# Kernel optimization log

Hardware: AMD Instinct MI355X
Metric: run time of the kernel (lower is better)

Reference implementation:

```python
import jax, jax.numpy as jnp
import numpy as np

HIDDEN = 4096
N_HEADS = 8
HEAD = HIDDEN // N_HEADS  # 512
SCALE = float(HIDDEN) ** 0.5  # NOTE: module MULTIPLIES by sqrt(hidden_dim), faithful to source
NEG = -1e9


def setup_inputs() -> dict:
    key = jax.random.key(0)
    ks = jax.random.split(key, 7)
    B, S = 4, 2048
    q = jax.random.normal(ks[0], (B, S, HIDDEN), dtype=jnp.float32)
    k = jax.random.normal(ks[1], (B, S, HIDDEN), dtype=jnp.float32)
    v = jax.random.normal(ks[2], (B, S, HIDDEN), dtype=jnp.float32)
    mask = jax.random.randint(ks[3], (B, S), 0, 2, dtype=jnp.int32)
    w_std = 1.0 / np.sqrt(HIDDEN)
    Wq = jax.random.normal(ks[4], (HEAD, HIDDEN), dtype=jnp.float32) * w_std
    Wk = jax.random.normal(ks[5], (HEAD, HIDDEN), dtype=jnp.float32) * w_std
    Wv = jax.random.normal(ks[6], (HEAD, HIDDEN), dtype=jnp.float32) * w_std
    return {"q": q, "k": k, "v": v, "mask": mask, "Wq": Wq, "Wk": Wk, "Wv": Wv}


def reference(q, k, v, mask, Wq, Wk, Wv):
    # bias-free linear projections (nn.Linear: x @ W.T)
    qh = jnp.einsum('bse,de->bsd', q, Wq)  # [B,S,HEAD]
    kh = jnp.einsum('bse,de->bsd', k, Wk)
    vh = jnp.einsum('bse,de->bsd', v, Wv)
    # scores: q @ k^T, then MULTIPLY by sqrt(hidden_dim) as in source
    scores = jnp.einsum('bsd,btd->bst', qh, kh) * SCALE  # [B,S,S]
    # additive mask over keys: mask [B,S] -> [B,1,S]; done under no_grad in torch
    scores = jnp.where(mask[:, None, :] == 0, NEG, scores)
    scores = jax.lax.stop_gradient(scores)  # torch no_grad reassignment detaches
    attn = jax.nn.softmax(scores, axis=-1)
    # dropout p=0.0 -> identity
    out = jnp.einsum('bst,btd->bsd', attn, vh)  # [B,S,HEAD]
    return out
```

## Files before the change

kernel.cpp:

```cpp
#include <hip/hip_runtime.h>

#define HIDDEN 4096
#define HEADD  512
#define SEQ    2048
#define NBATCH 4
#define KSPLIT 4
#define KRANGE (SEQ/KSPLIT)
#define KSTR   520

typedef float f32x4 __attribute__((ext_vector_type(4)));
typedef short s16x8 __attribute__((ext_vector_type(8)));

__device__ __forceinline__ unsigned short f2bf(float x){
  unsigned u = __float_as_uint(x);
  u += 0x7fffu + ((u >> 16) & 1u);
  return (unsigned short)(u >> 16);
}
__device__ __forceinline__ float bf2f(unsigned short b){
  return __uint_as_float(((unsigned)b) << 16);
}
__device__ __forceinline__ void gl_lds16(const unsigned short* g, unsigned short* l){
  __builtin_amdgcn_global_load_lds((const __attribute__((address_space(1))) unsigned int*)g,
                                   (__attribute__((address_space(3))) unsigned int*)l,
                                   16, 0, 0);
}

__global__ void wsplit_kernel(const float* __restrict__ Wq,
                              const float* __restrict__ Wk,
                              const float* __restrict__ Wv,
                              unsigned short* __restrict__ wqh, unsigned short* __restrict__ wql,
                              unsigned short* __restrict__ wkh, unsigned short* __restrict__ wkl,
                              unsigned short* __restrict__ wvh){
  const int n4 = HEADD * HIDDEN / 4;
  for (int i = blockIdx.x * blockDim.x + threadIdx.x; i < n4; i += gridDim.x * blockDim.x){
    float4 a = ((const float4*)Wq)[i];
    ushort4 h, lo;
    h.x = f2bf(a.x); lo.x = f2bf(a.x - bf2f(h.x));
    h.y = f2bf(a.y); lo.y = f2bf(a.y - bf2f(h.y));
    h.z = f2bf(a.z); lo.z = f2bf(a.z - bf2f(h.z));
    h.w = f2bf(a.w); lo.w = f2bf(a.w - bf2f(h.w));
    ((ushort4*)wqh)[i] = h; ((ushort4*)wql)[i] = lo;
    a = ((const float4*)Wk)[i];
    h.x = f2bf(a.x); lo.x = f2bf(a.x - bf2f(h.x));
    h.y = f2bf(a.y); lo.y = f2bf(a.y - bf2f(h.y));
    h.z = f2bf(a.z); lo.z = f2bf(a.z - bf2f(h.z));
    h.w = f2bf(a.w); lo.w = f2bf(a.w - bf2f(h.w));
    ((ushort4*)wkh)[i] = h; ((ushort4*)wkl)[i] = lo;
    a = ((const float4*)Wv)[i];
    h.x = f2bf(a.x); h.y = f2bf(a.y); h.z = f2bf(a.z); h.w = f2bf(a.w);
    ((ushort4*)wvh)[i] = h;
  }
}

__global__ __launch_bounds__(512, 4)
void proj_all_kernel(const float* __restrict__ q, const float* __restrict__ k,
                     const float* __restrict__ v,
                     const unsigned short* __restrict__ wqh, const unsigned short* __restrict__ wql,
                     const unsigned short* __restrict__ wkh, const unsigned short* __restrict__ wkl,
                     const unsigned short* __restrict__ wvh,
                     unsigned short* __restrict__ qhh, unsigned short* __restrict__ qhl,
                     unsigned short* __restrict__ khh, unsigned short* __restrict__ khl,
                     unsigned short* __restrict__ vhT){
  __shared__ unsigned short Ah[2][128*32];
  __shared__ unsigned short Al[2*128*32];
  __shared__ unsigned short Bh[2][128*32];
  __shared__ unsigned short Bl[2*128*32];

  const int tid  = threadIdx.x;
  const int lane = tid & 63, wid = tid >> 6;
  const int quad = lane >> 4, l16 = lane & 15;
  const int wm = wid >> 1, wn = wid & 1;

  const int wg  = blockIdx.x + 4 * blockIdx.y + 256 * blockIdx.z;
  const int lwg = (wg & 7) * 96 + (wg >> 3);
  const int n0 = (lwg & 3) * 128;
  const int m0 = ((lwg >> 2) & 63) * 128;
  const int z  = lwg >> 8;

  const float* X = (z == 0) ? q : (z == 1) ? k : v;
  const unsigned short* Wh = (z == 0) ? wqh : (z == 1) ? wkh : wvh;
  const unsigned short* Wl = (z == 0) ? wql : (z == 1) ? wkl : wvh;
  unsigned short* Ohi = (z == 0) ? qhh : khh;
  unsigned short* Olo = (z == 0) ? qhl : khl;
  const bool full = (z < 2);

  const int sB    = (lane & 7) ^ (lane >> 3);
  const int browS = ((lane >> 3) << 1) + (sB >> 2);
  const int bcolS = (sB & 3) << 3;

  const int fbase = ((l16 >> 1) << 6) + ((((((l16 & 1) << 2) | quad)) ^ (l16 >> 1)) << 3);

  f32x4 acc[2][4];
  #pragma unroll
  for (int i = 0; i < 2; i++)
    #pragma unroll
    for (int j = 0; j < 4; j++){
      f32x4 zz = {0.f, 0.f, 0.f, 0.f};
      acc[i][j] = zz;
    }

  float4 xa[4];
  int ar[4], ahalf[4], acin[4], aidx[4];
  #pragma unroll
  for (int c = 0; c < 4; c++){
    int chunk = tid + c * 512;
    ar[c]    = chunk >> 4;
    int col4 = (chunk & 15) << 2;
    ahalf[c] = col4 >> 5;
    acin[c]  = col4 & 31;
    int R  = ar[c] >> 1;
    int sA = (((ar[c] & 1) << 2) | (acin[c] >> 3)) ^ (R & 7);
    aidx[c] = (R << 6) + (sA << 3) + (acin[c] & 7);
    xa[c] = *(const float4*)(X + (size_t)(m0 + ar[c]) * HIDDEN + col4);
  }

  for (int k0 = 0; k0 < HIDDEN; k0 += 64){
    #pragma unroll
    for (int c = 0; c < 4; c++){
      ushort4 hv;
      hv.x = f2bf(xa[c].x); hv.y = f2bf(xa[c].y); hv.z = f2bf(xa[c].z); hv.w = f2bf(xa[c].w);
      *(ushort4*)(&Ah[ahalf[c]][aidx[c]]) = hv;
      if (full){
        ushort4 lv;
        lv.x = f2bf(xa[c].x - bf2f(hv.x));
        lv.y = f2bf(xa[c].y - bf2f(hv.y));
        lv.z = f2bf(xa[c].z - bf2f(hv.z));
        lv.w = f2bf(xa[c].w - bf2f(hv.w));
        *(ushort4*)(&Al[ahalf[c]*4096 + aidx[c]]) = lv;
      }
    }
    #pragma unroll
    for (int h = 0; h < 2; h++){
      const unsigned short* gh = Wh + (size_t)(n0 + wid*16 + browS) * HIDDEN + k0 + h*32 + bcolS;
      gl_lds16(gh, &Bh[h][wid*512]);
      if (full){
        const unsigned short* gl = Wl + (size_t)(n0 + wid*16 + browS) * HIDDEN + k0 + h*32 + bcolS;
        gl_lds16(gl, &Bl[h*4096 + wid*512]);
      }
    }
    __syncthreads();
    if (k0 + 64 < HIDDEN){
      #pragma unroll
      for (int c = 0; c < 4; c++){
        int col4 = ahalf[c]*32 + acin[c];
        xa[c] = *(const float4*)(X + (size_t)(m0 + ar[c]) * HIDDEN + k0 + 64 + col4);
      }
    }
    #pragma unroll
    for (int h = 0; h < 2; h++){
      s16x8 ah[2], al[2], bh[4], bl[4];
      #pragma unroll
      for (int i = 0; i < 2; i++){
        ah[i] = *(const s16x8*)(&Ah[h][(wm*32 + i*16)*32 + fbase]);
        if (full) al[i] = *(const s16x8*)(&Al[h*4096 + (wm*32 + i*16)*32 + fbase]);
      }
      #pragma unroll
      for (int j = 0; j < 4; j++){
        bh[j] = *(const s16x8*)(&Bh[h][(wn*64 + j*16)*32 + fbase]);
        if (full) bl[j] = *(const s16x8*)(&Bl[h*4096 + (wn*64 + j*16)*32 + fbase]);
      }
      #pragma unroll
      for (int i = 0; i < 2; i++)
        #pragma unroll
        for (int j = 0; j < 4; j++){
          acc[i][j] = __builtin_amdgcn_mfma_f32_16x16x32_bf16(ah[i], bh[j], acc[i][j], 0, 0, 0);
          if (full){
            acc[i][j] = __builtin_amdgcn_mfma_f32_16x16x32_bf16(ah[i], bl[j], acc[i][j], 0, 0, 0);
            acc[i][j] = __builtin_amdgcn_mfma_f32_16x16x32_bf16(al[i], bh[j], acc[i][j], 0, 0, 0);
          }
        }
    }
    __syncthreads();
  }

  if (full){
    #pragma unroll
    for (int i = 0; i < 2; i++)
      #pragma unroll
      for (int j = 0; j < 4; j++)
        #pragma unroll
        for (int r = 0; r < 4; r++){
          int m = m0 + wm*32 + i*16 + quad*4 + r;
          int n = n0 + wn*64 + j*16 + l16;
          float c = acc[i][j][r];
          unsigned short h = f2bf(c);
          Ohi[(size_t)m * HEADD + n] = h;
          Olo[(size_t)m * HEADD + n] = f2bf(c - bf2f(h));
        }
  } else {
    #pragma unroll
    for (int i = 0; i < 2; i++)
      #pragma unroll
      for (int j = 0; j < 4; j++){
        int mbase = m0 + wm*32 + i*16 + quad*4;
        int d = n0 + wn*64 + j*16 + l16;
        int b = mbase >> 11;
        int t = mbase & 2047;
        ushort4 vv;
        vv.x = f2bf(acc[i][j][0]);
        vv.y = f2bf(acc[i][j][1]);
        vv.z = f2bf(acc[i][j][2]);
        vv.w = f2bf(acc[i][j][3]);
        *(ushort4*)(vhT + ((size_t)(b * HEADD + d)) * SEQ + t) = vv;
      }
  }
}

__global__ __launch_bounds__(512, 2)
void flash_kernel(const unsigned short* __restrict__ qhh, const unsigned short* __restrict__ qhl,
                  const unsigned short* __restrict__ khh, const unsigned short* __restrict__ khl,
                  const unsigned short* __restrict__ vhT, const int* __restrict__ mask,
                  float* __restrict__ part, float* __restrict__ ml){
  __shared__ unsigned short Kh[32*KSTR];
  __shared__ unsigned short Kl[32*KSTR];
  __shared__ unsigned short Vt[512*32];
  __shared__ unsigned short Pt[8*512];

  const int tid = threadIdx.x, lane = tid & 63, wid = tid >> 6;
  const int quad = lane >> 4, l16 = lane & 15;

  const int wg  = blockIdx.x + (int)gridDim.x * (blockIdx.y + (int)gridDim.y * blockIdx.z);
  const int lwg = (wg & 7) * 32 + (wg >> 3);
  const int qt = lwg & 15;
  const int kz = (lwg >> 4) & 3;
  const int b  = lwg >> 6;
  const int qrow0 = qt * 128 + wid * 16;
  const int kbase = kz * KRANGE;

  const int sV   = (lane & 7) ^ (lane >> 3);
  const int vdro = ((lane >> 3) << 1) + (sV >> 2);
  const int vcol = (sV & 3) << 3;
  const int vbase = ((l16 >> 1) << 6) + ((((((l16 & 1) << 2) | quad)) ^ (l16 >> 1)) << 3);

  const size_t qoff = ((size_t)(b * SEQ) + qrow0 + l16) * HEADD + quad * 8;
  s16x8 qh[16];
  #pragma unroll
  for (int ds = 0; ds < 16; ds++) qh[ds] = *(const s16x8*)(qhh + qoff + ds*32);

  float mrow[4], lrow[4];
  #pragma unroll
  for (int r = 0; r < 4; r++){ mrow[r] = -3.0e38f; lrow[r] = 0.f; }
  f32x4 oacc[32];
  #pragma unroll
  for (int j = 0; j < 32; j++){
    f32x4 z = {0.f, 0.f, 0.f, 0.f};
    oacc[j] = z;
  }

  auto stageK = [&](int kt){
    #pragma unroll
    for (int c = 0; c < 4; c++){
      int keyl = wid*4 + c;
      size_t g = ((size_t)(b * SEQ) + kbase + kt + keyl) * HEADD + lane*8;
      gl_lds16(khh + g, Kh + keyl*KSTR);
      gl_lds16(khl + g, Kl + keyl*KSTR);
    }
  };
  auto stageV = [&](int kt){
    #pragma unroll
    for (int c = 0; c < 4; c++){
      int d0 = wid*64 + c*16;
      const unsigned short* vs = vhT + ((size_t)(b * HEADD) + d0 + vdro) * SEQ
                                     + kbase + kt + vcol;
      gl_lds16(vs, Vt + d0*32);
    }
  };

  stageK(0);
  stageV(0);
  __syncthreads();

  for (int kt = 0; kt < KRANGE; kt += 32){
    const bool has_next = (kt + 32 < KRANGE);
    const int key0 = kbase + kt + l16;
    const int mk0 = mask[b * SEQ + key0];
    const int mk1 = mask[b * SEQ + key0 + 16];

    f32x4 s0 = {0.f,0.f,0.f,0.f}, s1 = {0.f,0.f,0.f,0.f};
    #pragma unroll
    for (int ds = 0; ds < 16; ds++){
      s16x8 aL  = *(const s16x8*)(qhl + qoff + ds*32);
      s16x8 b0H = *(const s16x8*)(Kh + l16*KSTR      + ds*32 + quad*8);
      s16x8 b0L = *(const s16x8*)(Kl + l16*KSTR      + ds*32 + quad*8);
      s16x8 b1H = *(const s16x8*)(Kh + (16+l16)*KSTR + ds*32 + quad*8);
      s16x8 b1L = *(const s16x8*)(Kl + (16+l16)*KSTR + ds*32 + quad*8);
      s0 = __builtin_amdgcn_mfma_f32_16x16x32_bf16(qh[ds], b0H, s0, 0, 0, 0);
      s0 = __builtin_amdgcn_mfma_f32_16x16x32_bf16(qh[ds], b0L, s0, 0, 0, 0);
      s0 = __builtin_amdgcn_mfma_f32_16x16x32_bf16(aL,     b0H, s0, 0, 0, 0);
      s0 = __builtin_amdgcn_mfma_f32_16x16x32_bf16(aL,     b0L, s0, 0, 0, 0);
      s1 = __builtin_amdgcn_mfma_f32_16x16x32_bf16(qh[ds], b1H, s1, 0, 0, 0);
      s1 = __builtin_amdgcn_mfma_f32_16x16x32_bf16(qh[ds], b1L, s1, 0, 0, 0);
      s1 = __builtin_amdgcn_mfma_f32_16x16x32_bf16(aL,     b1H, s1, 0, 0, 0);
      s1 = __builtin_amdgcn_mfma_f32_16x16x32_bf16(aL,     b1L, s1, 0, 0, 0);
    }

    __syncthreads();

    if (has_next) stageK(kt + 32);

    float sm0[4], sm1[4];
    #pragma unroll
    for (int r = 0; r < 4; r++){
      sm0[r] = mk0 ? s0[r] * 64.0f : -1.0e9f;
      sm1[r] = mk1 ? s1[r] * 64.0f : -1.0e9f;
    }
    float rm[4];
    #pragma unroll
    for (int r = 0; r < 4; r++) rm[r] = fmaxf(sm0[r], sm1[r]);
    #pragma unroll
    for (int sh = 1; sh < 16; sh <<= 1){
      #pragma unroll
      for (int r = 0; r < 4; r++) rm[r] = fmaxf(rm[r], __shfl_xor(rm[r], sh, 64));
    }
    bool needv = false;
    #pragma unroll
    for (int r = 0; r < 4; r++) needv = needv || (rm[r] > mrow[r] + 10.0f);
    const bool dorescale = (__any(needv ? 1 : 0) != 0);
    float alpha[4];
    if (dorescale){
      #pragma unroll
      for (int r = 0; r < 4; r++){
        float mn = fmaxf(mrow[r], rm[r]);
        alpha[r] = __expf(mrow[r] - mn);
        mrow[r] = mn;
      }
    } else {
      #pragma unroll
      for (int r = 0; r < 4; r++) alpha[r] = 1.0f;
    }
    float p0[4], p1[4], rs[4];
    #pragma unroll
    for (int r = 0; r < 4; r++){
      p0[r] = __expf(sm0[r] - mrow[r]);
      p1[r] = __expf(sm1[r] - mrow[r]);
      rs[r] = p0[r] + p1[r];
    }
    #pragma unroll
    for (int sh = 1; sh < 16; sh <<= 1){
      #pragma unroll
      for (int r = 0; r < 4; r++) rs[r] += __shfl_xor(rs[r], sh, 64);
    }
    #pragma unroll
    for (int r = 0; r < 4; r++) lrow[r] = lrow[r] * alpha[r] + rs[r];
    #pragma unroll
    for (int r = 0; r < 4; r++){
      Pt[wid*512 + (quad*4 + r)*32 + l16]      = f2bf(p0[r]);
      Pt[wid*512 + (quad*4 + r)*32 + 16 + l16] = f2bf(p1[r]);
    }
    if (dorescale){
      #pragma unroll
      for (int j = 0; j < 32; j++)
        #pragma unroll
        for (int r = 0; r < 4; r++) oacc[j][r] *= alpha[r];
    }
    s16x8 pa = *(const s16x8*)(Pt + wid*512 + l16*32 + quad*8);
    #pragma unroll
    for (int j = 0; j < 32; j++){
      s16x8 vb = *(const s16x8*)(Vt + j*512 + vbase);
      oacc[j] = __builtin_amdgcn_mfma_f32_16x16x32_bf16(pa, vb, oacc[j], 0, 0, 0);
    }

    __syncthreads();

    if (has_next) stageV(kt + 32);
  }

  const size_t prow = (size_t)(kz * (NBATCH*SEQ)) + b * SEQ + qrow0;
  #pragma unroll
  for (int j = 0; j < 32; j++)
    #pragma unroll
    for (int r = 0; r < 4; r++)
      part[(prow + quad*4 + r) * HEADD + j*16 + l16] = oacc[j][r];
  if (l16 == 0){
    #pragma unroll
    for (int r = 0; r < 4; r++){
      ml[(prow + quad*4 + r)*2 + 0] = mrow[r];
      ml[(prow + quad*4 + r)*2 + 1] = lrow[r];
    }
  }
}

__global__ __launch_bounds__(256)
void reduce_kernel(const float* __restrict__ part, const float* __restrict__ ml,
                   float* __restrict__ out){
  const int row = blockIdx.x;
  const int t = threadIdx.x;
  float m[KSPLIT], l[KSPLIT];
  float M = -3.0e38f;
  #pragma unroll
  for (int j = 0; j < KSPLIT; j++){
    m[j] = ml[((size_t)j*(NBATCH*SEQ) + row)*2 + 0];
    l[j] = ml[((size_t)j*(NBATCH*SEQ) + row)*2 + 1];
    M = fmaxf(M, m[j]);
  }
  float w[KSPLIT], L = 0.f;
  #pragma unroll
  for (int j = 0; j < KSPLIT; j++){
    w[j] = __expf(m[j] - M);
    L += w[j] * l[j];
  }
  const float invL = 1.0f / L;
  #pragma unroll
  for (int c = 0; c < 2; c++){
    int d = t + c*256;
    float acc = 0.f;
    #pragma unroll
    for (int j = 0; j < KSPLIT; j++)
      acc += w[j] * part[((size_t)j*(NBATCH*SEQ) + row)*HEADD + d];
    out[(size_t)row * HEADD + d] = acc * invL;
  }
}

extern "C" void kernel_launch(void* const* d_in, const int* in_sizes, int n_in,
                              void* d_out, int out_size, void* d_ws, size_t ws_size,
                              hipStream_t stream){
  const float* q    = (const float*)d_in[0];
  const float* k    = (const float*)d_in[1];
  const float* v    = (const float*)d_in[2];
  const int*   mask = (const int*)d_in[3];
  const float* Wq   = (const float*)d_in[4];
  const float* Wk   = (const float*)d_in[5];
  const float* Wv   = (const float*)d_in[6];
  float* out = (float*)d_out;

  char* ws = (char*)d_ws;
  const size_t MB = 1024 * 1024;
  unsigned short* wqh = (unsigned short*)(ws + 0*MB);
  unsigned short* wql = (unsigned short*)(ws + 4*MB);
  unsigned short* wkh = (unsigned short*)(ws + 8*MB);
  unsigned short* wkl = (unsigned short*)(ws + 12*MB);
  unsigned short* wvh = (unsigned short*)(ws + 16*MB);
  unsigned short* qhh = (unsigned short*)(ws + 20*MB);
  unsigned short* qhl = (unsigned short*)(ws + 28*MB);
  unsigned short* khh = (unsigned short*)(ws + 36*MB);
  unsigned short* khl = (unsigned short*)(ws + 44*MB);
  unsigned short* vhT = (unsigned short*)(ws + 52*MB);
  float*          part = (float*)(ws + 60*MB);
  float*          mlb  = (float*)(ws + 124*MB);

  hipLaunchKernelGGL(wsplit_kernel, dim3(1024), dim3(256), 0, stream,
                     Wq, Wk, Wv, wqh, wql, wkh, wkl, wvh);
  hipLaunchKernelGGL(proj_all_kernel, dim3(4, 64, 3), dim3(512), 0, stream,
                     q, k, v, wqh, wql, wkh, wkl, wvh, qhh, qhl, khh, khl, vhT);
  hipLaunchKernelGGL(flash_kernel, dim3(SEQ/128, KSPLIT, NBATCH), dim3(512), 0, stream,
                     qhh, qhl, khh, khl, vhT, mask, part, mlb);
  hipLaunchKernelGGL(reduce_kernel, dim3(NBATCH*SEQ), dim3(256), 0, stream,
                     part, mlb, out);
}
```

Before: 839.2 us.

## Halve projection K-tile to raise occupancy and always rescale softmax accumulator

The projection kernel now processes K in steps of 32 instead of 64. That halves its shared-memory tiles and staging registers, and the launch bound is raised to 6 blocks per CU so more workgroups can be resident. In exchange there are twice as many barrier-separated iterations with less MFMA work between them. The attention kernel drops the lazy-rescale threshold check and always rescales the output accumulator, which removes a wave vote and branch but adds 128 multiplies per tile.

```diff
diff --git a/kernel.cpp b/kernel.cpp
--- a/kernel.cpp
+++ b/kernel.cpp
@@ -52,7 +52,7 @@
   }
 }
 
-__global__ __launch_bounds__(512, 4)
+__global__ __launch_bounds__(512, 6)
 void proj_all_kernel(const float* __restrict__ q, const float* __restrict__ k,
                      const float* __restrict__ v,
                      const unsigned short* __restrict__ wqh, const unsigned short* __restrict__ wql,
@@ -61,10 +61,10 @@
                      unsigned short* __restrict__ qhh, unsigned short* __restrict__ qhl,
                      unsigned short* __restrict__ khh, unsigned short* __restrict__ khl,
                      unsigned short* __restrict__ vhT){
-  __shared__ unsigned short Ah[2][128*32];
-  __shared__ unsigned short Al[2*128*32];
-  __shared__ unsigned short Bh[2][128*32];
-  __shared__ unsigned short Bl[2*128*32];
+  __shared__ unsigned short Ah[128*32];
+  __shared__ unsigned short Al[128*32];
+  __shared__ unsigned short Bh[128*32];
+  __shared__ unsigned short Bl[128*32];
 
   const int tid  = threadIdx.x;
   const int lane = tid & 63, wid = tid >> 6;
@@ -99,65 +99,60 @@
       acc[i][j] = zz;
     }
 
-  float4 xa[4];
-  int ar[4], ahalf[4], acin[4], aidx[4];
-  #pragma unroll
-  for (int c = 0; c < 4; c++){
+  float4 xa[2];
+  int ar[2], acin[2], aidx[2];
+  #pragma unroll
+  for (int c = 0; c < 2; c++){
     int chunk = tid + c * 512;
-    ar[c]    = chunk >> 4;
-    int col4 = (chunk & 15) << 2;
-    ahalf[c] = col4 >> 5;
-    acin[c]  = col4 & 31;
+    ar[c]    = chunk >> 3;
+    int col4 = (chunk & 7) << 2;
+    acin[c]  = col4;
     int R  = ar[c] >> 1;
-    int sA = (((ar[c] & 1) << 2) | (acin[c] >> 3)) ^ (R & 7);
-    aidx[c] = (R << 6) + (sA << 3) + (acin[c] & 7);
+    int sA = (((ar[c] & 1) << 2) | (col4 >> 3)) ^ (R & 7);
+    aidx[c] = (R << 6) + (sA << 3) + (col4 & 7);
     xa[c] = *(const float4*)(X + (size_t)(m0 + ar[c]) * HIDDEN + col4);
   }
 
-  for (int k0 = 0; k0 < HIDDEN; k0 += 64){
-    #pragma unroll
-    for (int c = 0; c < 4; c++){
+  for (int k0 = 0; k0 < HIDDEN; k0 += 32){
+    #pragma unroll
+    for (int c = 0; c < 2; c++){
       ushort4 hv;
       hv.x = f2bf(xa[c].x); hv.y = f2bf(xa[c].y); hv.z = f2bf(xa[c].z); hv.w = f2bf(xa[c].w);
-      *(ushort4*)(&Ah[ahalf[c]][aidx[c]]) = hv;
+      *(ushort4*)(&Ah[aidx[c]]) = hv;
       if (full){
         ushort4 lv;
         lv.x = f2bf(xa[c].x - bf2f(hv.x));
         lv.y = f2bf(xa[c].y - bf2f(hv.y));
         lv.z = f2bf(xa[c].z - bf2f(hv.z));
         lv.w = f2bf(xa[c].w - bf2f(hv.w));
-        *(ushort4*)(&Al[ahalf[c]*4096 + aidx[c]]) = lv;
+        *(ushort4*)(&Al[aidx[c]]) = lv;
       }
     }
-    #pragma unroll
-    for (int h = 0; h < 2; h++){
-      const unsigned short* gh = Wh + (size_t)(n0 + wid*16 + browS) * HIDDEN + k0 + h*32 + bcolS;
-      gl_lds16(gh, &Bh[h][wid*512]);
+    {
+      const unsigned short* gh = Wh + (size_t)(n0 + wid*16 + browS) * HIDDEN + k0 + bcolS;
+      gl_lds16(gh, &Bh[wid*512]);
       if (full){
-        const unsigned short* gl = Wl + (size_t)(n0 + wid*16 + browS) * HIDDEN + k0 + h*32 + bcolS;
-        gl_lds16(gl, &Bl[h*4096 + wid*512]);
+        const unsigned short* gl = Wl + (size_t)(n0 + wid*16 + browS) * HIDDEN + k0 + bcolS;
+        gl_lds16(gl, &Bl[wid*512]);
       }
     }
     __syncthreads();
-    if (k0 + 64 < HIDDEN){
-      #pragma unroll
-      for (int c = 0; c < 4; c++){
-        int col4 = ahalf[c]*32 + acin[c];
-        xa[c] = *(const float4*)(X + (size_t)(m0 + ar[c]) * HIDDEN + k0 + 64 + col4);
+    if (k0 + 32 < HIDDEN){
+      #pragma unroll
+      for (int c = 0; c < 2; c++)
+        xa[c] = *(const float4*)(X + (size_t)(m0 + ar[c]) * HIDDEN + k0 + 32 + acin[c]);
+    }
+    {
+      s16x8 ah[2], al[2], bh[4], bl[4];
+      #pragma unroll
+      for (int i = 0; i < 2; i++){
+        ah[i] = *(const s16x8*)(&Ah[(wm*32 + i*16)*32 + fbase]);
+        if (full) al[i] = *(const s16x8*)(&Al[(wm*32 + i*16)*32 + fbase]);
       }
-    }
-    #pragma unroll
-    for (int h = 0; h < 2; h++){
-      s16x8 ah[2], al[2], bh[4], bl[4];
-      #pragma unroll
-      for (int i = 0; i < 2; i++){
-        ah[i] = *(const s16x8*)(&Ah[h][(wm*32 + i*16)*32 + fbase]);
-        if (full) al[i] = *(const s16x8*)(&Al[h*4096 + (wm*32 + i*16)*32 + fbase]);
-      }
       #pragma unroll
       for (int j = 0; j < 4; j++){
-        bh[j] = *(const s16x8*)(&Bh[h][(wn*64 + j*16)*32 + fbase]);
-        if (full) bl[j] = *(const s16x8*)(&Bl[h*4096 + (wn*64 + j*16)*32 + fbase]);
+        bh[j] = *(const s16x8*)(&Bh[(wn*64 + j*16)*32 + fbase]);
+        if (full) bl[j] = *(const s16x8*)(&Bl[(wn*64 + j*16)*32 + fbase]);
       }
       #pragma unroll
       for (int i = 0; i < 2; i++)
@@ -312,27 +307,14 @@
       #pragma unroll
       for (int r = 0; r < 4; r++) rm[r] = fmaxf(rm[r], __shfl_xor(rm[r], sh, 64));
     }
-    bool needv = false;
-    #pragma unroll
-    for (int r = 0; r < 4; r++) needv = needv || (rm[r] > mrow[r] + 10.0f);
-    const bool dorescale = (__any(needv ? 1 : 0) != 0);
-    float alpha[4];
-    if (dorescale){
-      #pragma unroll
-      for (int r = 0; r < 4; r++){
-        float mn = fmaxf(mrow[r], rm[r]);
-        alpha[r] = __expf(mrow[r] - mn);
-        mrow[r] = mn;
-      }
-    } else {
-      #pragma unroll
-      for (int r = 0; r < 4; r++) alpha[r] = 1.0f;
-    }
-    float p0[4], p1[4], rs[4];
+    float alpha[4], p0[4], p1[4], rs[4];
     #pragma unroll
     for (int r = 0; r < 4; r++){
-      p0[r] = __expf(sm0[r] - mrow[r]);
-      p1[r] = __expf(sm1[r] - mrow[r]);
+      float mn = fmaxf(mrow[r], rm[r]);
+      alpha[r] = __expf(mrow[r] - mn);
+      mrow[r] = mn;
+      p0[r] = __expf(sm0[r] - mn);
+      p1[r] = __expf(sm1[r] - mn);
       rs[r] = p0[r] + p1[r];
     }
     #pragma unroll
@@ -347,12 +329,10 @@
       Pt[wid*512 + (quad*4 + r)*32 + l16]      = f2bf(p0[r]);
       Pt[wid*512 + (quad*4 + r)*32 + 16 + l16] = f2bf(p1[r]);
     }
-    if (dorescale){
-      #pragma unroll
-      for (int j = 0; j < 32; j++)
-        #pragma unroll
-        for (int r = 0; r < 4; r++) oacc[j][r] *= alpha[r];
-    }
+    #pragma unroll
+    for (int j = 0; j < 32; j++)
+      #pragma unroll
+      for (int r = 0; r < 4; r++) oacc[j][r] *= alpha[r];
     s16x8 pa = *(const s16x8*)(Pt + wid*512 + l16*32 + quad*8);
     #pragma unroll
     for (int j = 0; j < 32; j++){
```

Result: slower. 2.412 ms (+187.4%).
